# Kernel tuning notes

Measured on AMD Instinct MI355X. Metric: run time of the kernel, lower is better.

Reference implementation:

```python
import jax, jax.numpy as jnp
import numpy as np

DIM = 1024
H = 8
D = DIM // H
EPS = 1e-5


def setup_inputs() -> dict:
    key = jax.random.key(0)
    ks = jax.random.split(key, 12)
    B, T, Kt, Ka, Kp = 4, 2048, 64, 16, 32
    s = 1.0 / np.sqrt(DIM).astype(np.float32)
    return {
        "x": jax.random.normal(ks[0], (B, T, DIM), jnp.float32),
        "h_t": jax.random.normal(ks[1], (B, Kt, DIM), jnp.float32),
        "h_a": jax.random.normal(ks[2], (B, Ka, DIM), jnp.float32),
        "p": jax.random.normal(ks[3], (B, Kp, DIM), jnp.float32),
        "Wq": jax.random.normal(ks[4], (DIM, DIM), jnp.float32) * s,
        "bq": jnp.zeros((DIM,), jnp.float32),
        "Wk": jax.random.normal(ks[5], (DIM, DIM), jnp.float32) * s,
        "bk": jnp.zeros((DIM,), jnp.float32),
        "Wv": jax.random.normal(ks[6], (DIM, DIM), jnp.float32) * s,
        "bv": jnp.zeros((DIM,), jnp.float32),
        "Wo": jax.random.normal(ks[7], (DIM, DIM), jnp.float32) * s,
        "bo": jnp.zeros((DIM,), jnp.float32),
        "ln_g": jnp.ones((DIM,), jnp.float32),
        "ln_b": jnp.zeros((DIM,), jnp.float32),
        "Wf": jax.random.normal(ks[8], (DIM, DIM), jnp.float32) * s,
        "bf": jnp.zeros((DIM,), jnp.float32),
        "gating": jnp.zeros((1,), jnp.float32),
    }


def reference(x, h_t, h_a, p, Wq, bq, Wk, bk, Wv, bv, Wo, bo, ln_g, ln_b, Wf, bf, gating):
    B, T, C = x.shape
    ratio_g = jnp.tanh(gating)  # (1,), broadcasts over scores
    h_cond = jnp.concatenate([h_a, p], axis=1)  # [B, K_cond, C]

    def proj(t, W, b):
        # linear then split heads: [B, S, C] -> [B, H, S, D]
        y = t @ W + b
        return y.reshape(t.shape[0], t.shape[1], H, D).transpose(0, 2, 1, 3)

    q = proj(x, Wq, bq)
    k_tok, v_tok = proj(x, Wk, bk), proj(x, Wv, bv)
    k_task, v_task = proj(h_t, Wk, bk), proj(h_t, Wv, bv)
    k_cond, v_cond = proj(h_cond, Wk, bk), proj(h_cond, Wv, bv)

    s_tok = jnp.einsum('bhqd,bhkd->bhqk', q, k_tok)
    s_task = jnp.einsum('bhqd,bhkd->bhqk', q, k_task)
    s_cond = jnp.einsum('bhqd,bhkd->bhqk', q, k_cond) * ratio_g  # gated group
    scores = jnp.concatenate([s_tok, s_task, s_cond], axis=-1) / np.sqrt(D).astype(np.float32)
    w = jax.nn.softmax(scores, axis=-1)

    v_comb = jnp.concatenate([v_tok, v_task, v_cond], axis=2)  # [B, H, T+Kt+Kc, D]
    o = jnp.einsum('bhqk,bhkd->bhqd', w, v_comb).transpose(0, 2, 1, 3).reshape(B, T, C)
    o = o @ Wo + bo

    y = o + x  # residual feeds LN-MLP
    mu = jnp.mean(y, axis=-1, keepdims=True)
    var = jnp.var(y, axis=-1, keepdims=True)
    yn = (y - mu) / jnp.sqrt(var + EPS) * ln_g + ln_b
    return jax.nn.relu(yn @ Wf + bf)
```

## Files before the change

kernel.cpp:

```cpp
#include <hip/hip_runtime.h>
#include <hip/hip_bf16.h>

#define BB 4
#define TT 2048
#define CC 1024
#define HH 8
#define DD 128
#define KTOT 2160
#define GATE0 2112
#define KP 2176
#define NT 34
#define MQ (BB*TT)
#define MKVP (BB*KP)

typedef __attribute__((ext_vector_type(4)))  float f32x4;
typedef __attribute__((ext_vector_type(16))) float f32x16;
typedef __attribute__((ext_vector_type(8)))  short bf16x8;

union PU { unsigned u[4]; bf16x8 v; };

__device__ __forceinline__ unsigned short f2bf(float f) {
    unsigned u = __float_as_uint(f);
    unsigned r = u + 0x7FFFu + ((u >> 16) & 1u);
    return (unsigned short)(r >> 16);
}
__device__ __forceinline__ unsigned pk2(float a, float b) {
    unsigned r;
    asm("v_cvt_pk_bf16_f32 %0, %1, %2" : "=v"(r) : "v"(a), "v"(b));
    return r;
}
__device__ __forceinline__ float ex2(float x) {
    float r;
    asm("v_exp_f32 %0, %1" : "=v"(r) : "v"(x));
    return r;
}
__device__ __forceinline__ void async16(const ushort* g, ushort* l) {
    __builtin_amdgcn_global_load_lds((const __attribute__((address_space(1))) void*)g,
                                     (__attribute__((address_space(3))) void*)l, 16, 0, 0);
}

__global__ __launch_bounds__(256) void tcast5(const float* __restrict__ W0, const float* __restrict__ W1,
        const float* __restrict__ W2, const float* __restrict__ W3, const float* __restrict__ W4,
        ushort* __restrict__ D0, ushort* __restrict__ D1, ushort* __restrict__ D2,
        ushort* __restrict__ D3, ushort* __restrict__ D4, float alpha) {
    const float* W; ushort* Dt; float sc = 1.f;
    switch (blockIdx.z) {
        case 0:  W = W0; Dt = D0; sc = alpha; break;
        case 1:  W = W1; Dt = D1; break;
        case 2:  W = W2; Dt = D2; break;
        case 3:  W = W3; Dt = D3; break;
        default: W = W4; Dt = D4; break;
    }
    __shared__ float tile[32][33];
    const int tx = threadIdx.x & 31, ty = threadIdx.x >> 5;
    const int n0 = blockIdx.x * 32, k0 = blockIdx.y * 32;
    #pragma unroll
    for (int i = 0; i < 4; i++)
        tile[ty + i*8][tx] = W[(size_t)(k0 + ty + i*8)*CC + n0 + tx];
    __syncthreads();
    #pragma unroll
    for (int i = 0; i < 4; i++)
        Dt[(size_t)(n0 + ty + i*8)*CC + k0 + tx] = f2bf(tile[tx][ty + i*8] * sc);
}

__global__ __launch_bounds__(256) void gather_kv(const float* __restrict__ x, const float* __restrict__ ht,
        const float* __restrict__ ha, const float* __restrict__ p, ushort* __restrict__ kvb) {
    int idx = blockIdx.x * 256 + threadIdx.x;
    int col4 = idx & 255;
    int row  = idx >> 8;
    int b = row / KP, j = row - b * KP;
    ushort4 o;
    if (j < KTOT) {
        const float* src;
        if (j < 2048)      src = x  + ((size_t)b*TT + j)*CC;
        else if (j < 2112) src = ht + ((size_t)b*64 + (j-2048))*CC;
        else if (j < 2128) src = ha + ((size_t)b*16 + (j-2112))*CC;
        else               src = p  + ((size_t)b*32 + (j-2128))*CC;
        float4 v = ((const float4*)src)[col4];
        o.x = f2bf(v.x); o.y = f2bf(v.y); o.z = f2bf(v.z); o.w = f2bf(v.w);
    } else {
        o.x = 0; o.y = 0; o.z = 0; o.w = 0;
    }
    ((ushort4*)kvb)[idx] = o;
}

__global__ __launch_bounds__(256) void gemm_qkv(const ushort* __restrict__ A, const ushort* __restrict__ Wt,
        const float* __restrict__ bq, const float* __restrict__ bk, const float* __restrict__ bv,
        const float* __restrict__ gate, ushort* __restrict__ Qb, ushort* __restrict__ Kb,
        ushort* __restrict__ Vtb, float alpha) {
    __shared__ ushort As[128*64];
    __shared__ ushort Bs[128*64];
    const int t = threadIdx.x;
    const int w = t >> 6, lane = t & 63;
    const int wr = w >> 1, wc = w & 1;
    const int row0 = blockIdx.y * 128, col0 = blockIdx.x * 128;
    const int lr = lane & 15, ls = lane >> 4;
    const int cb = col0 >> 10;
    const int b_ = row0 / KP;
    const int jb = row0 - b_ * KP;
    const float ratio = tanhf(gate[0]);
    f32x4 acc[4][4] = {};
    for (int k0 = 0; k0 < CC; k0 += 64) {
        #pragma unroll
        for (int u = 0; u < 4; u++) {
            int i = u*256 + t;
            int r = i >> 3, sl = i & 7;
            int ss = sl ^ (r & 7);
            async16(A  + (size_t)(row0 + r)*CC + k0 + ss*8, &As[i*8]);
            async16(Wt + (size_t)(col0 + r)*CC + k0 + ss*8, &Bs[i*8]);
        }
        __syncthreads();
        #pragma unroll
        for (int ks = 0; ks < 2; ks++) {
            bf16x8 af[4], bg[4];
            #pragma unroll
            for (int mi = 0; mi < 4; mi++) {
                int row = wr*64 + mi*16 + lr;
                af[mi] = *(const bf16x8*)&As[row*64 + ((ks*4 + ls) ^ (row & 7))*8];
            }
            #pragma unroll
            for (int ni = 0; ni < 4; ni++) {
                int row = wc*64 + ni*16 + lr;
                bg[ni] = *(const bf16x8*)&Bs[row*64 + ((ks*4 + ls) ^ (row & 7))*8];
            }
            #pragma unroll
            for (int mi = 0; mi < 4; mi++)
                #pragma unroll
                for (int ni = 0; ni < 4; ni++)
                    acc[mi][ni] = __builtin_amdgcn_mfma_f32_16x16x32_bf16(af[mi], bg[ni], acc[mi][ni], 0, 0, 0);
        }
        __syncthreads();
    }
    #pragma unroll
    for (int ni = 0; ni < 4; ni++) {
        const int colw = (col0 & 1023) + wc*64 + ni*16 + lr;
        float bcol;
        if (cb == 0)      bcol = bq[colw] * alpha;
        else if (cb == 1) bcol = bk[colw];
        else              bcol = bv[colw];
        #pragma unroll
        for (int mi = 0; mi < 4; mi++) {
            f32x4 v = acc[mi][ni];
            #pragma unroll
            for (int q = 0; q < 4; q++) {
                int roff = wr*64 + mi*16 + ls*4 + q;
                int j = jb + roff;
                float o = v[q] + bcol;
                if (cb == 0) {
                    if (j < TT) Qb[(size_t)(b_*TT + j)*CC + colw] = f2bf(o);
                } else if (cb == 1) {
                    if (j >= GATE0) o *= ratio;
                    Kb[(size_t)(row0 + roff)*CC + colw] = f2bf(o);
                } else {
                    int hh = colw >> 7, dout = colw & 127;
                    Vtb[((size_t)((b_*HH + hh)*DD + dout))*KP + j] = f2bf(o);
                }
            }
        }
    }
}

template<int EPI>
__global__ __launch_bounds__(256) void gemm_mfma(const ushort* __restrict__ A, const ushort* __restrict__ Bt,
        const float* __restrict__ bias, const float* __restrict__ res, void* __restrict__ Cv) {
    __shared__ ushort As[128*64];
    __shared__ ushort Bs[128*64];
    const int t = threadIdx.x;
    const int w = t >> 6, lane = t & 63;
    const int wr = w >> 1, wc = w & 1;
    const int row0 = blockIdx.y * 128, col0 = blockIdx.x * 128;
    const int lr = lane & 15, ls = lane >> 4;
    f32x4 acc[4][4] = {};
    for (int k0 = 0; k0 < CC; k0 += 64) {
        #pragma unroll
        for (int u = 0; u < 4; u++) {
            int i = u*256 + t;
            int r = i >> 3, sl = i & 7;
            int ss = sl ^ (r & 7);
            async16(A  + (size_t)(row0 + r)*CC + k0 + ss*8, &As[i*8]);
            async16(Bt + (size_t)(col0 + r)*CC + k0 + ss*8, &Bs[i*8]);
        }
        __syncthreads();
        #pragma unroll
        for (int ks = 0; ks < 2; ks++) {
            bf16x8 af[4], bg[4];
            #pragma unroll
            for (int mi = 0; mi < 4; mi++) {
                int row = wr*64 + mi*16 + lr;
                af[mi] = *(const bf16x8*)&As[row*64 + ((ks*4 + ls) ^ (row & 7))*8];
            }
            #pragma unroll
            for (int ni = 0; ni < 4; ni++) {
                int row = wc*64 + ni*16 + lr;
                bg[ni] = *(const bf16x8*)&Bs[row*64 + ((ks*4 + ls) ^ (row & 7))*8];
            }
            #pragma unroll
            for (int mi = 0; mi < 4; mi++)
                #pragma unroll
                for (int ni = 0; ni < 4; ni++)
                    acc[mi][ni] = __builtin_amdgcn_mfma_f32_16x16x32_bf16(af[mi], bg[ni], acc[mi][ni], 0, 0, 0);
        }
        __syncthreads();
    }
    #pragma unroll
    for (int ni = 0; ni < 4; ni++) {
        const int col = col0 + wc*64 + ni*16 + lr;
        const float bcol = bias[col];
        #pragma unroll
        for (int mi = 0; mi < 4; mi++) {
            f32x4 v = acc[mi][ni];
            #pragma unroll
            for (int q = 0; q < 4; q++) {
                int row = row0 + wr*64 + mi*16 + ls*4 + q;
                float o = v[q] + bcol;
                if constexpr (EPI == 1) {
                    o += res[(size_t)row*CC + col];
                    ((ushort*)Cv)[(size_t)row*CC + col] = f2bf(o);
                } else {
                    o = fmaxf(o, 0.f);
                    ((float*)Cv)[(size_t)row*CC + col] = o;
                }
            }
        }
    }
}

__global__ __launch_bounds__(256, 2) void attn_mfma(const ushort* __restrict__ Qb,
        const ushort* __restrict__ Kb, const ushort* __restrict__ Vtb,
        ushort* __restrict__ AO) {
    __shared__ ushort s_k[2][64*128];
    __shared__ ushort s_v[2][64*128];
    __shared__ float  l_s[4][32];
    const int t = threadIdx.x;
    const int w = t >> 6, lane = t & 63;
    const int ql = lane & 31, H = lane >> 5;
    const int bid = blockIdx.x;
    const int h   = bid & 7;
    const int s_  = bid >> 3;
    const int b   = s_ & 3;
    const int qb0 = (s_ >> 2) * 128;

    #pragma unroll
    for (int u = 0; u < 8; u++) {
        int s16 = u*256 + t;
        int row = s16 >> 4, slot = s16 & 15;
        int ss = slot ^ (row & 15);
        const ushort* src = Qb + (size_t)(b*TT + qb0 + row)*CC + h*DD + ss*8;
        ushort* dst = (s16 < 1024) ? &s_k[0][s16*8] : &s_v[0][(s16 - 1024)*8];
        async16(src, dst);
    }
    asm volatile("s_waitcnt vmcnt(0)" ::: "memory");
    __builtin_amdgcn_s_barrier();
    bf16x8 qf[8];
    {
        int row = w*32 + ql;
        #pragma unroll
        for (int ds = 0; ds < 8; ds++) {
            int sp = (ds*2 + H) ^ (row & 15);
            const ushort* base = (row < 64) ? &s_k[0][row*128 + sp*8]
                                            : &s_v[0][(row-64)*128 + sp*8];
            qf[ds] = *(const bf16x8*)base;
        }
    }
    asm volatile("s_waitcnt lgkmcnt(0)" ::: "memory");
    __builtin_amdgcn_s_barrier();

    f32x16 oacc[4] = {};
    float m = -__builtin_inff(), l = 0.f;

    const size_t kbase = (size_t)(b*KP)*CC + h*DD;
    const size_t vbase = ((size_t)((b*HH + h)*DD))*KP;

    {
        #pragma unroll
        for (int u = 0; u < 4; u++) {
            int s16 = u*256 + t;
            int row = s16 >> 4, slot = s16 & 15;
            int ss = slot ^ (row & 15);
            async16(Kb + kbase + (size_t)row*CC + ss*8, &s_k[0][s16*8]);
        }
        #pragma unroll
        for (int u = 0; u < 4; u++) {
            int s16 = u*256 + t;
            int row = s16 >> 4, slot = s16 & 15;
            int ss = slot ^ (row & 15);
            int d = row + ((ss >> 3) << 6);
            int js = ss & 7;
            async16(Vtb + vbase + (size_t)d*KP + js*8, &s_v[0][s16*8]);
        }
    }

    for (int tile = 0; tile < NT; tile++) {
        const int cur = tile & 1;
        if (tile + 1 < NT) {
            const int j0n = (tile+1) * 64;
            #pragma unroll
            for (int u = 0; u < 4; u++) {
                int s16 = u*256 + t;
                int row = s16 >> 4, slot = s16 & 15;
                int ss = slot ^ (row & 15);
                async16(Kb + kbase + (size_t)(j0n + row)*CC + ss*8, &s_k[cur^1][s16*8]);
            }
            #pragma unroll
            for (int u = 0; u < 4; u++) {
                int s16 = u*256 + t;
                int row = s16 >> 4, slot = s16 & 15;
                int ss = slot ^ (row & 15);
                int d = row + ((ss >> 3) << 6);
                int js = ss & 7;
                async16(Vtb + vbase + (size_t)d*KP + j0n + js*8, &s_v[cur^1][s16*8]);
            }
            asm volatile("s_waitcnt vmcnt(8)" ::: "memory");
        } else {
            asm volatile("s_waitcnt vmcnt(0)" ::: "memory");
        }
        __builtin_amdgcn_s_barrier();

        const ushort* ks = s_k[cur];
        const ushort* vs = s_v[cur];

        f32x16 st0 = {}, st1 = {};
        #pragma unroll
        for (int ds = 0; ds < 8; ds++) {
            int g = ds*2 + H;
            bf16x8 k0 = *(const bf16x8*)&ks[ ql      *128 + (g ^ ( ql      & 15))*8];
            bf16x8 k1 = *(const bf16x8*)&ks[(32+ql)*128 + (g ^ ((32+ql) & 15))*8];
            st0 = __builtin_amdgcn_mfma_f32_32x32x16_bf16(k0, qf[ds], st0, 0, 0, 0);
            st1 = __builtin_amdgcn_mfma_f32_32x32x16_bf16(k1, qf[ds], st1, 0, 0, 0);
        }

        float p0[16], p1[16];
        if (tile == NT - 1) {
            #pragma unroll
            for (int r = 0; r < 16; r++) {
                int cr = (r&3) + 8*(r>>2) + 4*H;
                p0[r] = st0[r];
                p1[r] = (cr < 16) ? st1[r] : -__builtin_inff();
            }
        } else {
            #pragma unroll
            for (int r = 0; r < 16; r++) { p0[r] = st0[r]; p1[r] = st1[r]; }
        }

        float tm = -__builtin_inff();
        #pragma unroll
        for (int r = 0; r < 16; r++) tm = fmaxf(tm, fmaxf(p0[r], p1[r]));
        tm = fmaxf(tm, __shfl_xor(tm, 32));
        tm = fmaxf(tm, __shfl_xor(tm, 16));
        tm = fmaxf(tm, __shfl_xor(tm, 8));
        tm = fmaxf(tm, __shfl_xor(tm, 4));
        tm = fmaxf(tm, __shfl_xor(tm, 2));
        tm = fmaxf(tm, __shfl_xor(tm, 1));
        if (tm > m + 11.5f) {
            float rs = ex2(m - tm);
            m = tm;
            l *= rs;
            #pragma unroll
            for (int dt = 0; dt < 4; dt++)
                #pragma unroll
                for (int r = 0; r < 16; r++) oacc[dt][r] *= rs;
        }
        float lsum = 0.f;
        #pragma unroll
        for (int r = 0; r < 16; r++) {
            p0[r] = ex2(p0[r] - m);
            p1[r] = ex2(p1[r] - m);
            lsum += p0[r] + p1[r];
        }
        lsum += __shfl_xor(lsum, 32);
        l += lsum;

        #pragma unroll
        for (int jt = 0; jt < 4; jt++) {
            const float* ps = (jt < 2) ? p0 : p1;
            const int ib = (jt & 1) * 8;
            unsigned PA0 = pk2(ps[ib+0], ps[ib+1]);
            unsigned PA1 = pk2(ps[ib+2], ps[ib+3]);
            unsigned PB0 = pk2(ps[ib+4], ps[ib+5]);
            unsigned PB1 = pk2(ps[ib+6], ps[ib+7]);
            unsigned send0 = H ? PA0 : PB0;
            unsigned send1 = H ? PA1 : PB1;
            unsigned recv0 = (unsigned)__shfl_xor((int)send0, 32);
            unsigned recv1 = (unsigned)__shfl_xor((int)send1, 32);
            PU pu;
            pu.u[0] = H ? recv0 : PA0;
            pu.u[1] = H ? recv1 : PA1;
            pu.u[2] = H ? PB0  : recv0;
            pu.u[3] = H ? PB1  : recv1;
            #pragma unroll
            for (int dt = 0; dt < 4; dt++) {
                int d = dt*32 + ql;
                int row = d & 63;
                int g = ((d >> 6) << 3) + jt*2 + H;
                int sp = g ^ (row & 15);
                bf16x8 vf = *(const bf16x8*)&vs[row*128 + sp*8];
                oacc[dt] = __builtin_amdgcn_mfma_f32_32x32x16_bf16(pu.v, vf, oacc[dt], 0, 0, 0);
            }
        }
        asm volatile("" ::: "memory");
        __builtin_amdgcn_s_barrier();
    }

    l_s[w][ql] = 1.0f / l;
    __syncthreads();
    float il[16];
    #pragma unroll
    for (int r = 0; r < 16; r++) il[r] = l_s[w][(r&3) + 8*(r>>2) + 4*H];
    #pragma unroll
    for (int dt = 0; dt < 4; dt++)
        #pragma unroll
        for (int r = 0; r < 16; r++) {
            int cr = (r&3) + 8*(r>>2) + 4*H;
            size_t row = (size_t)(b*TT + qb0 + w*32 + cr);
            AO[row*CC + h*DD + dt*32 + ql] = f2bf(oacc[dt][r] * il[r]);
        }
}

__global__ __launch_bounds__(256) void ln_bf16(const ushort* __restrict__ Y, const float* __restrict__ g,
        const float* __restrict__ bb, ushort* __restrict__ Out) {
    const int row = blockIdx.x;
    const int t = threadIdx.x;
    ushort4 u4 = ((const ushort4*)(Y + (size_t)row*CC))[t];
    float v0 = __uint_as_float((unsigned)u4.x << 16);
    float v1 = __uint_as_float((unsigned)u4.y << 16);
    float v2 = __uint_as_float((unsigned)u4.z << 16);
    float v3 = __uint_as_float((unsigned)u4.w << 16);
    float s  = v0 + v1 + v2 + v3;
    float sq = v0*v0 + v1*v1 + v2*v2 + v3*v3;
    #pragma unroll
    for (int off = 32; off >= 1; off >>= 1) {
        s  += __shfl_xor(s, off);
        sq += __shfl_xor(sq, off);
    }
    __shared__ float ssum[4], ssq[4];
    const int w = t >> 6;
    if ((t & 63) == 0) { ssum[w] = s; ssq[w] = sq; }
    __syncthreads();
    s  = ssum[0] + ssum[1] + ssum[2] + ssum[3];
    sq = ssq[0]  + ssq[1]  + ssq[2]  + ssq[3];
    const float mu  = s * (1.f/1024.f);
    const float var = sq * (1.f/1024.f) - mu*mu;
    const float inv = rsqrtf(var + 1e-5f);
    float4 g4 = ((const float4*)g)[t];
    float4 b4 = ((const float4*)bb)[t];
    ushort4 o;
    o.x = f2bf((v0 - mu)*inv*g4.x + b4.x);
    o.y = f2bf((v1 - mu)*inv*g4.y + b4.y);
    o.z = f2bf((v2 - mu)*inv*g4.z + b4.z);
    o.w = f2bf((v3 - mu)*inv*g4.w + b4.w);
    ((ushort4*)(Out + (size_t)row*CC))[t] = o;
}

extern "C" void kernel_launch(void* const* d_in, const int* in_sizes, int n_in,
                              void* d_out, int out_size, void* d_ws, size_t ws_size,
                              hipStream_t stream) {
    const float* x    = (const float*)d_in[0];
    const float* h_t  = (const float*)d_in[1];
    const float* h_a  = (const float*)d_in[2];
    const float* p    = (const float*)d_in[3];
    const float* Wq   = (const float*)d_in[4];
    const float* bq   = (const float*)d_in[5];
    const float* Wk   = (const float*)d_in[6];
    const float* bk   = (const float*)d_in[7];
    const float* Wv   = (const float*)d_in[8];
    const float* bv   = (const float*)d_in[9];
    const float* Wo   = (const float*)d_in[10];
    const float* bo   = (const float*)d_in[11];
    const float* ln_g = (const float*)d_in[12];
    const float* ln_b = (const float*)d_in[13];
    const float* Wf   = (const float*)d_in[14];
    const float* bf   = (const float*)d_in[15];
    const float* gate = (const float*)d_in[16];
    float* out = (float*)d_out;

    const float alpha = 0.088388347648318447f * 1.4426950408889634f;

    ushort* wqT = (ushort*)d_ws;
    ushort* wkT = wqT + (size_t)CC*CC;
    ushort* wvT = wkT + (size_t)CC*CC;
    ushort* woT = wvT + (size_t)CC*CC;
    ushort* wfT = woT + (size_t)CC*CC;
    ushort* kvb = wfT + (size_t)CC*CC;
    ushort* Qb  = kvb + (size_t)MKVP*CC;
    ushort* Kb  = Qb  + (size_t)MQ*CC;
    ushort* Vtb = Kb  + (size_t)MKVP*CC;
    ushort* AOb = Vtb + (size_t)MKVP*CC;
    ushort* Yb  = Kb;
    ushort* YNb = kvb;

    tcast5<<<dim3(32,32,5), 256, 0, stream>>>(Wq, Wk, Wv, Wo, Wf, wqT, wkT, wvT, woT, wfT, alpha);
    gather_kv<<<MKVP, 256, 0, stream>>>(x, h_t, h_a, p, kvb);

    gemm_qkv<<<dim3(24, MKVP/128), 256, 0, stream>>>(kvb, wqT, bq, bk, bv, gate, Qb, Kb, Vtb, alpha);
    attn_mfma<<<dim3(512), 256, 0, stream>>>(Qb, Kb, Vtb, AOb);
    gemm_mfma<1><<<dim3(8, MQ/128), 256, 0, stream>>>(AOb, woT, bo, x, (void*)Yb);
    ln_bf16<<<MQ, 256, 0, stream>>>(Yb, ln_g, ln_b, YNb);
    gemm_mfma<2><<<dim3(8, MQ/128), 256, 0, stream>>>(YNb, wfT, bf, nullptr, (void*)out);
}
```

Baseline: 275.1 us.

## Rewrite QKV GEMM as 256x256 tile, 8-wave, double-buffered pipelined kernel

Replaces the 128x128, 4-wave QKV projection GEMM with a 256x256-tile kernel of 8 waves that double-buffers LDS. The next K-slice is prefetched in four quarter-chunks interleaved across four compute phases, with explicit vmcnt/lgkmcnt waits, barriers, and s_setprio raised around the MFMA bursts. The aim is to hide global-load latency behind MFMA work and raise operand reuse per tile. In exchange it uses 128KB of LDS, runs one block per CU, and launches fewer blocks (12x34), which can leave CUs idle on the tail wave.

```diff
diff --git a/kernel.cpp b/kernel.cpp
--- a/kernel.cpp
+++ b/kernel.cpp
@@ -84,53 +84,109 @@
     ((ushort4*)kvb)[idx] = o;
 }
 
-__global__ __launch_bounds__(256) void gemm_qkv(const ushort* __restrict__ A, const ushort* __restrict__ Wt,
+__global__ __launch_bounds__(512, 1) void gemm_qkv8(const ushort* __restrict__ A, const ushort* __restrict__ Wt,
         const float* __restrict__ bq, const float* __restrict__ bk, const float* __restrict__ bv,
         const float* __restrict__ gate, ushort* __restrict__ Qb, ushort* __restrict__ Kb,
         ushort* __restrict__ Vtb, float alpha) {
-    __shared__ ushort As[128*64];
-    __shared__ ushort Bs[128*64];
+    __shared__ ushort As[2][256*64];
+    __shared__ ushort Bs[2][256*64];
     const int t = threadIdx.x;
     const int w = t >> 6, lane = t & 63;
-    const int wr = w >> 1, wc = w & 1;
-    const int row0 = blockIdx.y * 128, col0 = blockIdx.x * 128;
+    const int wr = w >> 2, wc = w & 3;
     const int lr = lane & 15, ls = lane >> 4;
+    const int row0 = blockIdx.y * 256, col0 = blockIdx.x * 256;
     const int cb = col0 >> 10;
-    const int b_ = row0 / KP;
-    const int jb = row0 - b_ * KP;
     const float ratio = tanhf(gate[0]);
-    f32x4 acc[4][4] = {};
-    for (int k0 = 0; k0 < CC; k0 += 64) {
-        #pragma unroll
-        for (int u = 0; u < 4; u++) {
-            int i = u*256 + t;
-            int r = i >> 3, sl = i & 7;
+
+    auto stageA = [&](int buf, int kt, int h) {
+        #pragma unroll
+        for (int u = 0; u < 2; u++) {
+            int i = u*512 + t;
+            int r = h*128 + (i >> 3), sl = i & 7;
             int ss = sl ^ (r & 7);
-            async16(A  + (size_t)(row0 + r)*CC + k0 + ss*8, &As[i*8]);
-            async16(Wt + (size_t)(col0 + r)*CC + k0 + ss*8, &Bs[i*8]);
-        }
-        __syncthreads();
-        #pragma unroll
-        for (int ks = 0; ks < 2; ks++) {
-            bf16x8 af[4], bg[4];
-            #pragma unroll
-            for (int mi = 0; mi < 4; mi++) {
-                int row = wr*64 + mi*16 + lr;
-                af[mi] = *(const bf16x8*)&As[row*64 + ((ks*4 + ls) ^ (row & 7))*8];
-            }
-            #pragma unroll
-            for (int ni = 0; ni < 4; ni++) {
-                int row = wc*64 + ni*16 + lr;
-                bg[ni] = *(const bf16x8*)&Bs[row*64 + ((ks*4 + ls) ^ (row & 7))*8];
-            }
+            async16(A + (size_t)(row0 + r)*CC + kt*64 + ss*8, &As[buf][(size_t)(h*1024 + i)*8]);
+        }
+    };
+    auto stageB = [&](int buf, int kt, int h) {
+        #pragma unroll
+        for (int u = 0; u < 2; u++) {
+            int i = u*512 + t;
+            int r = h*128 + (i >> 3), sl = i & 7;
+            int ss = sl ^ (r & 7);
+            async16(Wt + (size_t)(col0 + r)*CC + kt*64 + ss*8, &Bs[buf][(size_t)(h*1024 + i)*8]);
+        }
+    };
+
+    f32x4 acc[8][4] = {};
+
+    stageA(0, 0, 0); stageA(0, 0, 1); stageB(0, 0, 0); stageB(0, 0, 1);
+
+    for (int kt = 0; kt < 16; kt++) {
+        const int buf = kt & 1;
+        const bool pre = (kt + 1 < 16);
+        #pragma unroll
+        for (int ph = 0; ph < 4; ph++) {
+            const int q1 = ph >> 1, q2 = ph & 1;
+            bf16x8 af[4][2], bg[2][2];
+            if (ph == 0) {
+                if (pre) {
+                    stageA(buf ^ 1, kt + 1, 0);
+                    asm volatile("s_waitcnt vmcnt(2)" ::: "memory");
+                } else {
+                    asm volatile("s_waitcnt vmcnt(0)" ::: "memory");
+                }
+                __builtin_amdgcn_s_barrier();
+                #pragma unroll
+                for (int mi = 0; mi < 4; mi++) {
+                    int row = wr*128 + q1*64 + mi*16 + lr;
+                    #pragma unroll
+                    for (int ks = 0; ks < 2; ks++)
+                        af[mi][ks] = *(const bf16x8*)&As[buf][row*64 + ((ks*4 + ls) ^ (row & 7))*8];
+                }
+                #pragma unroll
+                for (int ni = 0; ni < 2; ni++) {
+                    int row = wc*64 + q2*32 + ni*16 + lr;
+                    #pragma unroll
+                    for (int ks = 0; ks < 2; ks++)
+                        bg[ni][ks] = *(const bf16x8*)&Bs[buf][row*64 + ((ks*4 + ls) ^ (row & 7))*8];
+                }
+            } else {
+                #pragma unroll
+                for (int mi = 0; mi < 4; mi++) {
+                    int row = wr*128 + q1*64 + mi*16 + lr;
+                    #pragma unroll
+                    for (int ks = 0; ks < 2; ks++)
+                        af[mi][ks] = *(const bf16x8*)&As[buf][row*64 + ((ks*4 + ls) ^ (row & 7))*8];
+                }
+                #pragma unroll
+                for (int ni = 0; ni < 2; ni++) {
+                    int row = wc*64 + q2*32 + ni*16 + lr;
+                    #pragma unroll
+                    for (int ks = 0; ks < 2; ks++)
+                        bg[ni][ks] = *(const bf16x8*)&Bs[buf][row*64 + ((ks*4 + ls) ^ (row & 7))*8];
+                }
+                if (pre) {
+                    if (ph == 1)      stageA(buf ^ 1, kt + 1, 1);
+                    else if (ph == 2) stageB(buf ^ 1, kt + 1, 0);
+                    else              stageB(buf ^ 1, kt + 1, 1);
+                }
+                __builtin_amdgcn_s_barrier();
+            }
+            asm volatile("s_waitcnt lgkmcnt(0)" ::: "memory");
+            __builtin_amdgcn_s_setprio(1);
             #pragma unroll
             for (int mi = 0; mi < 4; mi++)
                 #pragma unroll
-                for (int ni = 0; ni < 4; ni++)
-                    acc[mi][ni] = __builtin_amdgcn_mfma_f32_16x16x32_bf16(af[mi], bg[ni], acc[mi][ni], 0, 0, 0);
-        }
-        __syncthreads();
-    }
+                for (int ni = 0; ni < 2; ni++)
+                    #pragma unroll
+                    for (int ks = 0; ks < 2; ks++)
+                        acc[q1*4 + mi][q2*2 + ni] = __builtin_amdgcn_mfma_f32_16x16x32_bf16(
+                            af[mi][ks], bg[ni][ks], acc[q1*4 + mi][q2*2 + ni], 0, 0, 0);
+            __builtin_amdgcn_s_setprio(0);
+            __builtin_amdgcn_s_barrier();
+        }
+    }
+
     #pragma unroll
     for (int ni = 0; ni < 4; ni++) {
         const int colw = (col0 & 1023) + wc*64 + ni*16 + lr;
@@ -139,18 +195,21 @@
         else if (cb == 1) bcol = bk[colw];
         else              bcol = bv[colw];
         #pragma unroll
-        for (int mi = 0; mi < 4; mi++) {
+        for (int mi = 0; mi < 8; mi++) {
+            const int rbase = row0 + wr*128 + mi*16;
+            const int b_ = rbase / KP;
+            const int jb = rbase - b_ * KP;
             f32x4 v = acc[mi][ni];
             #pragma unroll
             for (int q = 0; q < 4; q++) {
-                int roff = wr*64 + mi*16 + ls*4 + q;
+                int roff = ls*4 + q;
                 int j = jb + roff;
                 float o = v[q] + bcol;
                 if (cb == 0) {
                     if (j < TT) Qb[(size_t)(b_*TT + j)*CC + colw] = f2bf(o);
                 } else if (cb == 1) {
                     if (j >= GATE0) o *= ratio;
-                    Kb[(size_t)(row0 + roff)*CC + colw] = f2bf(o);
+                    Kb[(size_t)(rbase + roff)*CC + colw] = f2bf(o);
                 } else {
                     int hh = colw >> 7, dout = colw & 127;
                     Vtb[((size_t)((b_*HH + hh)*DD + dout))*KP + j] = f2bf(o);
@@ -491,7 +550,7 @@
     tcast5<<<dim3(32,32,5), 256, 0, stream>>>(Wq, Wk, Wv, Wo, Wf, wqT, wkT, wvT, woT, wfT, alpha);
     gather_kv<<<MKVP, 256, 0, stream>>>(x, h_t, h_a, p, kvb);
 
-    gemm_qkv<<<dim3(24, MKVP/128), 256, 0, stream>>>(kvb, wqT, bq, bk, bv, gate, Qb, Kb, Vtb, alpha);
+    gemm_qkv8<<<dim3(12, MKVP/256), 512, 0, stream>>>(kvb, wqT, bq, bk, bv, gate, Qb, Kb, Vtb, alpha);
     attn_mfma<<<dim3(512), 256, 0, stream>>>(Qb, Kb, Vtb, AOb);
     gemm_mfma<1><<<dim3(8, MQ/128), 256, 0, stream>>>(AOb, woT, bo, x, (void*)Yb);
     ln_bf16<<<MQ, 256, 0, stream>>>(Yb, ln_g, ln_b, YNb);
```

Measured after the change: 284.3 us. 3.3% more time.
